# Optimization experiments

Measured on AMD Instinct MI355X. Metric: run time of the kernel, lower is better.

## Reference

```python
import jax, jax.numpy as jnp
import numpy as np

N_NODES = 100000
N_EDGES = 3200000


def gcn_conv(x, edge_index, W, b, n_nodes):
    # PyG GCNConv default: add self-loops, symmetric degree normalization,
    # linear transform, scatter-add aggregation at target nodes, add bias.
    src = jnp.concatenate([edge_index[0], jnp.arange(n_nodes, dtype=edge_index.dtype)])
    dst = jnp.concatenate([edge_index[1], jnp.arange(n_nodes, dtype=edge_index.dtype)])
    deg = jax.ops.segment_sum(jnp.ones_like(dst, dtype=x.dtype), dst, num_segments=n_nodes)
    dinv = jnp.where(deg > 0, jax.lax.rsqrt(jnp.maximum(deg, 1e-12)), 0.0)
    norm = dinv[src] * dinv[dst]            # [E+N]
    h = x @ W                               # [N, F_out]
    msg = h[src] * norm[:, None]            # gather + scale
    out = jax.ops.segment_sum(msg, dst, num_segments=n_nodes)
    return out + b


def setup_inputs() -> dict:
    key = jax.random.key(0)
    k1, k2, k3, k4 = jax.random.split(key, 4)
    x = jax.random.normal(k1, (N_NODES, 2), dtype=jnp.float32)
    edge_index = jax.random.randint(k2, (2, N_EDGES), 0, N_NODES, dtype=jnp.int64)
    # Glorot-ish init for weights, zero bias (PyG default zeros bias).
    W1 = jax.random.normal(k3, (2, 16), dtype=jnp.float32) * (1.0 / np.sqrt(2.0))
    b1 = jnp.zeros((16,), dtype=jnp.float32)
    W2 = jax.random.normal(k4, (16, 2), dtype=jnp.float32) * (1.0 / np.sqrt(16.0))
    b2 = jnp.zeros((2,), dtype=jnp.float32)
    return {"x": x, "edge_index": edge_index, "W1": W1, "b1": b1, "W2": W2, "b2": b2}


def reference(x, edge_index, W1, b1, W2, b2):
    n = x.shape[0]
    h = gcn_conv(x, edge_index, W1, b1, n)
    h = jax.nn.relu(h)
    h = gcn_conv(h, edge_index, W2, b2, n)
    return jax.nn.log_softmax(h, axis=1)
```

## Files before the change

### kernel.cpp

```cpp
#include <hip/hip_runtime.h>
#include <math.h>


#define BLK 256
#define NTILE 512
#define EPTMAX 6400
#define MAXB 512
#define MSK 0x1FFFFu
#define SRTMAX 10240


__global__ void k_hist(const int* __restrict__ dst, int* __restrict__ table,
                       int e, int ept, int nbkt) {
    __shared__ int h[MAXB];
    int tile = blockIdx.x;
    for (int i = threadIdx.x; i < MAXB; i += BLK) h[i] = 0;
    __syncthreads();
    int lo = tile * ept;
    int hi = min(lo + ept, e);
    for (int i = lo + 4 * threadIdx.x; i < hi; i += 4 * BLK) {
        int4 d4 = *(const int4*)(dst + i);
        atomicAdd(&h[d4.x >> 8], 1);
        atomicAdd(&h[d4.y >> 8], 1);
        atomicAdd(&h[d4.z >> 8], 1);
        atomicAdd(&h[d4.w >> 8], 1);
    }
    __syncthreads();
    for (int i = threadIdx.x; i < nbkt; i += BLK)
        table[tile * nbkt + i] = h[i];
}

__global__ void k_scan_col(int* __restrict__ table, int* __restrict__ tot, int nbkt) {
    __shared__ int wsum[NTILE / 64];
    int b = blockIdx.x;
    int t = threadIdx.x;
    int v = table[t * nbkt + b];
    int x = v;
    int lane = t & 63;
#pragma unroll
    for (int ofs = 1; ofs < 64; ofs <<= 1) {
        int y = __shfl_up(x, ofs, 64);
        if (lane >= ofs) x += y;
    }
    if (lane == 63) wsum[t >> 6] = x;
    __syncthreads();
    if (t < NTILE / 64) {
        int s = wsum[t];
        int w = s;
#pragma unroll
        for (int ofs = 1; ofs < NTILE / 64; ofs <<= 1) {
            int y = __shfl_up(w, ofs, 64);
            if (t >= ofs) w += y;
        }
        wsum[t] = w - s;
    }
    __syncthreads();
    int incl = x + wsum[t >> 6];
    table[t * nbkt + b] = incl - v;
    if (t == NTILE - 1) tot[b] = incl;
}

__global__ void k_scan_tot(const int* __restrict__ tot, int* __restrict__ bkt_off, int nbkt) {
    __shared__ int wsum[MAXB / 64];
    int t = threadIdx.x;
    int v = (t < nbkt) ? tot[t] : 0;
    int x = v;
    int lane = t & 63;
#pragma unroll
    for (int ofs = 1; ofs < 64; ofs <<= 1) {
        int y = __shfl_up(x, ofs, 64);
        if (lane >= ofs) x += y;
    }
    if (lane == 63) wsum[t >> 6] = x;
    __syncthreads();
    if (t < MAXB / 64) {
        int s = wsum[t];
        int w = s;
#pragma unroll
        for (int ofs = 1; ofs < MAXB / 64; ofs <<= 1) {
            int y = __shfl_up(w, ofs, 64);
            if (t >= ofs) w += y;
        }
        wsum[t] = w - s;
    }
    __syncthreads();
    int incl = x + wsum[t >> 6];
    if (t < nbkt) bkt_off[t] = incl - v;
    if (t == nbkt - 1) bkt_off[nbkt] = incl;
}

__global__ void k_scatter(const int* __restrict__ src, const int* __restrict__ dst,
                          const int* __restrict__ table, const int* __restrict__ tot,
                          const int* __restrict__ bkt_off, unsigned* __restrict__ sorted,
                          int e, int ept, int nbkt) {
    __shared__ int cur[MAXB];
    __shared__ int base2[MAXB];
    __shared__ unsigned stage[EPTMAX];
    __shared__ unsigned short stage_b[EPTMAX];
    __shared__ int wpart[BLK / 64];
    int tile = blockIdx.x;
    int t = threadIdx.x;
    int lo = tile * ept;
    int hi = min(lo + ept, e);
    int total = hi - lo;

    int b0 = 2 * t, b1 = 2 * t + 1;
    int c0 = 0, c1 = 0, g0 = 0, g1 = 0;
    if (b0 < nbkt) {
        int base = table[tile * nbkt + b0];
        int next = (tile < NTILE - 1) ? table[(tile + 1) * nbkt + b0] : tot[b0];
        c0 = next - base;
        g0 = bkt_off[b0] + base;
    }
    if (b1 < nbkt) {
        int base = table[tile * nbkt + b1];
        int next = (tile < NTILE - 1) ? table[(tile + 1) * nbkt + b1] : tot[b1];
        c1 = next - base;
        g1 = bkt_off[b1] + base;
    }
    int p = c0 + c1;
    int x = p;
    int lane = t & 63;
#pragma unroll
    for (int ofs = 1; ofs < 64; ofs <<= 1) {
        int y = __shfl_up(x, ofs, 64);
        if (lane >= ofs) x += y;
    }
    if (lane == 63) wpart[t >> 6] = x;
    __syncthreads();
    if (t < BLK / 64) {
        int s = wpart[t];
        int w = s;
#pragma unroll
        for (int ofs = 1; ofs < BLK / 64; ofs <<= 1) {
            int y = __shfl_up(w, ofs, 64);
            if (t >= ofs) w += y;
        }
        wpart[t] = w - s;
    }
    __syncthreads();
    int E = x + wpart[t >> 6] - p;
    cur[b0] = E;
    cur[b1] = E + c0;
    if (b0 < nbkt) base2[b0] = g0 - E;
    if (b1 < nbkt) base2[b1] = g1 - (E + c0);
    __syncthreads();

    for (int i = lo + 4 * t; i < hi; i += 4 * BLK) {
        int4 s4 = *(const int4*)(src + i);
        int4 d4 = *(const int4*)(dst + i);
        int b, pos;
        b = d4.x >> 8; pos = atomicAdd(&cur[b], 1);
        stage[pos] = (unsigned)s4.x | ((unsigned)(d4.x & 255) << 17); stage_b[pos] = (unsigned short)b;
        b = d4.y >> 8; pos = atomicAdd(&cur[b], 1);
        stage[pos] = (unsigned)s4.y | ((unsigned)(d4.y & 255) << 17); stage_b[pos] = (unsigned short)b;
        b = d4.z >> 8; pos = atomicAdd(&cur[b], 1);
        stage[pos] = (unsigned)s4.z | ((unsigned)(d4.z & 255) << 17); stage_b[pos] = (unsigned short)b;
        b = d4.w >> 8; pos = atomicAdd(&cur[b], 1);
        stage[pos] = (unsigned)s4.w | ((unsigned)(d4.w & 255) << 17); stage_b[pos] = (unsigned short)b;
    }
    __syncthreads();
    for (int j = t; j < total; j += BLK) {
        int b = stage_b[j];
        sorted[base2[b] + j] = stage[j];
    }
}

__global__ __launch_bounds__(256) void k_cnt(
        const unsigned* __restrict__ sorted, const int* __restrict__ bkt_off,
        const float* __restrict__ x, float* __restrict__ dinv,
        float* __restrict__ xp, int* __restrict__ nodeoff, int n, int nbkt) {
    __shared__ int cnt[256];
    __shared__ int wsum[4];
    int b = blockIdx.x, t = threadIdx.x;
    cnt[t] = 0;
    __syncthreads();
    int lo = bkt_off[b], hi = bkt_off[b + 1];
    int la = lo & ~3;
    for (int i = la + 4 * t; i < hi; i += 4 * 256) {
        uint4 r = *(const uint4*)(sorted + i);
        if (i >= lo && i + 4 <= hi) {
            atomicAdd(&cnt[r.x >> 17], 1);
            atomicAdd(&cnt[r.y >> 17], 1);
            atomicAdd(&cnt[r.z >> 17], 1);
            atomicAdd(&cnt[r.w >> 17], 1);
        } else {
            if (i + 0 >= lo && i + 0 < hi) atomicAdd(&cnt[r.x >> 17], 1);
            if (i + 1 >= lo && i + 1 < hi) atomicAdd(&cnt[r.y >> 17], 1);
            if (i + 2 >= lo && i + 2 < hi) atomicAdd(&cnt[r.z >> 17], 1);
            if (i + 3 >= lo && i + 3 < hi) atomicAdd(&cnt[r.w >> 17], 1);
        }
    }
    __syncthreads();
    int c = cnt[t];
    int node = (b << 8) + t;
    if (node < n) {
        float d = rsqrtf((float)c + 1.0f);
        dinv[node] = d;
        float2 xv = ((const float2*)x)[node];
        ((float2*)xp)[node] = make_float2(d * xv.x, d * xv.y);
    }
    int xsc = c;
    int lane = t & 63;
#pragma unroll
    for (int ofs = 1; ofs < 64; ofs <<= 1) {
        int y = __shfl_up(xsc, ofs, 64);
        if (lane >= ofs) xsc += y;
    }
    if (lane == 63) wsum[t >> 6] = xsc;
    __syncthreads();
    if (t < 4) {
        int s = wsum[t];
        int w = s;
#pragma unroll
        for (int ofs = 1; ofs < 4; ofs <<= 1) {
            int y = __shfl_up(w, ofs, 64);
            if (t >= ofs) w += y;
        }
        wsum[t] = w - s;
    }
    __syncthreads();
    int excl = xsc + wsum[t >> 6] - c;
    nodeoff[node] = lo + excl;
    if (b == nbkt - 1 && t == 255) nodeoff[node + 1] = hi;
}

__global__ __launch_bounds__(1024) void k_sagg1(
        const unsigned* __restrict__ sorted, const int* __restrict__ bkt_off,
        const int* __restrict__ nodeoff, const float* __restrict__ xp,
        const float* __restrict__ dinv, const float* __restrict__ W1,
        const float* __restrict__ b1, const float* __restrict__ W2,
        float* __restrict__ gp, unsigned* __restrict__ nsorted, int n) {
    __shared__ unsigned srt[SRTMAX];
    __shared__ int cur[256];
    __shared__ int stt[257];
    int b = blockIdx.x, t = threadIdx.x;
    int lo = bkt_off[b], hi = bkt_off[b + 1];
    if (t < 256) {
        int s = nodeoff[(b << 8) + t] - lo;
        cur[t] = s;
        stt[t] = s;
        if (t == 255) stt[256] = hi - lo;
    }
    __syncthreads();
    int la = lo & ~3;
    for (int i = la + 4 * t; i < hi; i += 4 * 1024) {
        uint4 r = *(const uint4*)(sorted + i);
        if (i >= lo && i + 4 <= hi) {
            int p0 = atomicAdd(&cur[r.x >> 17], 1); unsigned v0 = r.x & MSK; srt[p0] = v0; nsorted[lo + p0] = v0;
            int p1 = atomicAdd(&cur[r.y >> 17], 1); unsigned v1 = r.y & MSK; srt[p1] = v1; nsorted[lo + p1] = v1;
            int p2 = atomicAdd(&cur[r.z >> 17], 1); unsigned v2 = r.z & MSK; srt[p2] = v2; nsorted[lo + p2] = v2;
            int p3 = atomicAdd(&cur[r.w >> 17], 1); unsigned v3 = r.w & MSK; srt[p3] = v3; nsorted[lo + p3] = v3;
        } else {
            if (i + 0 >= lo && i + 0 < hi) { int p0 = atomicAdd(&cur[r.x >> 17], 1); unsigned v0 = r.x & MSK; srt[p0] = v0; nsorted[lo + p0] = v0; }
            if (i + 1 >= lo && i + 1 < hi) { int p1 = atomicAdd(&cur[r.y >> 17], 1); unsigned v1 = r.y & MSK; srt[p1] = v1; nsorted[lo + p1] = v1; }
            if (i + 2 >= lo && i + 2 < hi) { int p2 = atomicAdd(&cur[r.z >> 17], 1); unsigned v2 = r.z & MSK; srt[p2] = v2; nsorted[lo + p2] = v2; }
            if (i + 3 >= lo && i + 3 < hi) { int p3 = atomicAdd(&cur[r.w >> 17], 1); unsigned v3 = r.w & MSK; srt[p3] = v3; nsorted[lo + p3] = v3; }
        }
    }
    __syncthreads();

    int nl = t >> 2, q = t & 3;
    int gid = (b << 8) + nl;
    int s = stt[nl], epos = stt[nl + 1];
    const float2* xp2 = (const float2*)xp;
    float sx = 0.f, sy = 0.f;
    for (int p = s + q; p < epos; p += 4) {
        float2 f = xp2[srt[p]];
        sx += f.x; sy += f.y;
    }
    sx += __shfl_xor(sx, 1); sy += __shfl_xor(sy, 1);
    sx += __shfl_xor(sx, 2); sy += __shfl_xor(sy, 2);
    if (q == 0 && gid < n) {
        float d = dinv[gid];
        float2 xv = xp2[gid];
        float ax = d * (sx + xv.x), ay = d * (sy + xv.y);
        float g0 = 0.f, g1 = 0.f;
#pragma unroll
        for (int f = 0; f < 16; ++f) {
            float h = fmaf(ax, W1[f], fmaf(ay, W1[16 + f], b1[f]));
            h = fmaxf(h, 0.0f);
            g0 = fmaf(h, W2[2 * f + 0], g0);
            g1 = fmaf(h, W2[2 * f + 1], g1);
        }
        ((float2*)gp)[gid] = make_float2(d * g0, d * g1);
    }
}

__global__ void k_agg2(const unsigned* __restrict__ nsorted, const int* __restrict__ nodeoff,
                       const float* __restrict__ gp, const float* __restrict__ dinv,
                       const float* __restrict__ b2, float* __restrict__ out, int n) {
    int t = threadIdx.x;
    int nd = (blockIdx.x << 8) + (blockIdx.y << 6) + (t >> 2);
    int q = t & 3;
    if (nd >= n) return;
    int start = nodeoff[nd], end = nodeoff[nd + 1];
    const float2* gp2 = (const float2*)gp;
    float sx = 0.f, sy = 0.f;
    for (int p = (start & ~3) + 4 * q; p < end; p += 16) {
        uint4 r = *(const uint4*)(nsorted + p);
        if (p >= start && p + 4 <= end) {
            float2 f0 = gp2[r.x], f1 = gp2[r.y], f2 = gp2[r.z], f3 = gp2[r.w];
            sx += (f0.x + f1.x) + (f2.x + f3.x);
            sy += (f0.y + f1.y) + (f2.y + f3.y);
        } else {
            if (p + 0 >= start && p + 0 < end) { float2 f = gp2[r.x]; sx += f.x; sy += f.y; }
            if (p + 1 >= start && p + 1 < end) { float2 f = gp2[r.y]; sx += f.x; sy += f.y; }
            if (p + 2 >= start && p + 2 < end) { float2 f = gp2[r.z]; sx += f.x; sy += f.y; }
            if (p + 3 >= start && p + 3 < end) { float2 f = gp2[r.w]; sx += f.x; sy += f.y; }
        }
    }
    sx += __shfl_xor(sx, 1); sy += __shfl_xor(sy, 1);
    sx += __shfl_xor(sx, 2); sy += __shfl_xor(sy, 2);
    if (q == 0) {
        float d = dinv[nd];
        float2 gv = gp2[nd];
        float z0 = d * (sx + gv.x) + b2[0];
        float z1 = d * (sy + gv.y) + b2[1];
        float m = fmaxf(z0, z1);
        float lse = m + logf(expf(z0 - m) + expf(z1 - m));
        ((float2*)out)[nd] = make_float2(z0 - lse, z1 - lse);
    }
}

extern "C" void kernel_launch(void* const* d_in, const int* in_sizes, int n_in,
                              void* d_out, int out_size, void* d_ws, size_t ws_size,
                              hipStream_t stream) {
    const float* x  = (const float*)d_in[0];
    const int*   ei = (const int*)d_in[1];
    const float* W1 = (const float*)d_in[2];
    const float* b1 = (const float*)d_in[3];
    const float* W2 = (const float*)d_in[4];
    const float* b2 = (const float*)d_in[5];
    float* out = (float*)d_out;

    const int n = in_sizes[0] / 2;
    const int e = in_sizes[1] / 2;
    const int* src = ei;
    const int* dst = ei + e;

    const int nbkt = (n + 255) >> 8;
    int ept = (((e + NTILE - 1) / NTILE) + 3) & ~3;

    char* base = (char*)d_ws;
    size_t off = 0;
    auto take = [&](size_t bytes) { char* p = base + off; off += (bytes + 255) & ~(size_t)255; return p; };
    unsigned* sorted  = (unsigned*)take(((size_t)e + 8) * 4);
    int*      table   = (int*)take((size_t)NTILE * nbkt * 4);
    int*      tot     = (int*)take((size_t)MAXB * 4);
    int*      bkt_off = (int*)take((size_t)(MAXB + 1) * 4);
    unsigned* nsorted = (unsigned*)take(((size_t)e + 8) * 4);
    int*      nodeoff = (int*)take((size_t)(nbkt * 256 + 64) * 4);
    float*    dinv    = (float*)take((size_t)n * 4);
    float*    xp      = (float*)take((size_t)n * 8);
    float*    gp      = (float*)take((size_t)n * 8);

    dim3 gagg(nbkt, 4);

    k_hist    <<<NTILE, BLK, 0, stream>>>(dst, table, e, ept, nbkt);
    k_scan_col<<<nbkt, NTILE, 0, stream>>>(table, tot, nbkt);
    k_scan_tot<<<1, MAXB, 0, stream>>>(tot, bkt_off, nbkt);
    k_scatter <<<NTILE, BLK, 0, stream>>>(src, dst, table, tot, bkt_off, sorted, e, ept, nbkt);
    k_cnt     <<<nbkt, 256, 0, stream>>>(sorted, bkt_off, x, dinv, xp, nodeoff, n, nbkt);
    k_sagg1   <<<nbkt, 1024, 0, stream>>>(sorted, bkt_off, nodeoff, xp, dinv, W1, b1, W2, gp, nsorted, n);
    k_agg2    <<<gagg, BLK, 0, stream>>>(nsorted, nodeoff, gp, dinv, b2, out, n);
}
```

Measured before the change: 154.3 us.

## Fuse count, layer-1 and layer-2 aggregation into one cooperative kernel

Replaces the three final kernels (degree count, first aggregation with MLP, second aggregation with log-softmax) with one cooperative kernel that uses grid-wide syncs between phases. The per-bucket node-sorted neighbor list stays in shared memory across both layers, so the nsorted global buffer and its re-read are no longer needed, and two kernel launches go away. In exchange it needs all ~391 blocks of 1024 threads to be co-resident and pays for two grid barriers. If the cooperative launch fails it falls back to the old three-kernel path.

```diff
diff --git a/kernel.cpp b/kernel.cpp
--- a/kernel.cpp
+++ b/kernel.cpp
@@ -1,5 +1,8 @@
 #include <hip/hip_runtime.h>
+#include <hip/hip_cooperative_groups.h>
 #include <math.h>
+
+namespace cg = cooperative_groups;
 
 
 #define BLK 256
@@ -165,6 +168,146 @@
         sorted[base2[b] + j] = stage[j];
     }
 }
+
+__global__ __launch_bounds__(1024, 8) void k_fused(
+        const unsigned* __restrict__ sorted, const int* __restrict__ bkt_off,
+        const float* __restrict__ x, float* __restrict__ xp, float* __restrict__ gp,
+        const float* __restrict__ W1, const float* __restrict__ b1,
+        const float* __restrict__ W2, const float* __restrict__ b2,
+        float* __restrict__ out, int n) {
+    __shared__ unsigned srt[SRTMAX];
+    __shared__ int cnt[256];
+    __shared__ int stt[257];
+    __shared__ float dv[256];
+    __shared__ int wsum[4];
+    cg::grid_group grid = cg::this_grid();
+
+    int b = blockIdx.x, t = threadIdx.x;
+    int lo = bkt_off[b], hi = bkt_off[b + 1];
+    if (t < 256) cnt[t] = 0;
+    __syncthreads();
+    int la = lo & ~3;
+
+    for (int i = la + 4 * t; i < hi; i += 4096) {
+        uint4 r = *(const uint4*)(sorted + i);
+        if (i >= lo && i + 4 <= hi) {
+            atomicAdd(&cnt[r.x >> 17], 1);
+            atomicAdd(&cnt[r.y >> 17], 1);
+            atomicAdd(&cnt[r.z >> 17], 1);
+            atomicAdd(&cnt[r.w >> 17], 1);
+        } else {
+            if (i + 0 >= lo && i + 0 < hi) atomicAdd(&cnt[r.x >> 17], 1);
+            if (i + 1 >= lo && i + 1 < hi) atomicAdd(&cnt[r.y >> 17], 1);
+            if (i + 2 >= lo && i + 2 < hi) atomicAdd(&cnt[r.z >> 17], 1);
+            if (i + 3 >= lo && i + 3 < hi) atomicAdd(&cnt[r.w >> 17], 1);
+        }
+    }
+    __syncthreads();
+
+    int c = (t < 256) ? cnt[t] : 0;
+    if (t < 256) {
+        float d = rsqrtf((float)c + 1.0f);
+        dv[t] = d;
+        int node = (b << 8) + t;
+        if (node < n) {
+            float2 xv = ((const float2*)x)[node];
+            ((float2*)xp)[node] = make_float2(d * xv.x, d * xv.y);
+        }
+    }
+    int xsc = c;
+    int lane = t & 63;
+#pragma unroll
+    for (int ofs = 1; ofs < 64; ofs <<= 1) {
+        int y = __shfl_up(xsc, ofs, 64);
+        if (lane >= ofs) xsc += y;
+    }
+    if (t < 256 && lane == 63) wsum[t >> 6] = xsc;
+    __syncthreads();
+    if (t < 4) {
+        int s = wsum[t];
+        int w = s;
+#pragma unroll
+        for (int ofs = 1; ofs < 4; ofs <<= 1) {
+            int y = __shfl_up(w, ofs, 64);
+            if (t >= ofs) w += y;
+        }
+        wsum[t] = w - s;
+    }
+    __syncthreads();
+    if (t < 256) {
+        int excl = xsc + wsum[t >> 6] - c;
+        cnt[t] = excl;
+        stt[t] = excl;
+        if (t == 255) stt[256] = hi - lo;
+    }
+    __syncthreads();
+
+    for (int i = la + 4 * t; i < hi; i += 4096) {
+        uint4 r = *(const uint4*)(sorted + i);
+        if (i >= lo && i + 4 <= hi) {
+            int p0 = atomicAdd(&cnt[r.x >> 17], 1); srt[p0] = r.x & MSK;
+            int p1 = atomicAdd(&cnt[r.y >> 17], 1); srt[p1] = r.y & MSK;
+            int p2 = atomicAdd(&cnt[r.z >> 17], 1); srt[p2] = r.z & MSK;
+            int p3 = atomicAdd(&cnt[r.w >> 17], 1); srt[p3] = r.w & MSK;
+        } else {
+            if (i + 0 >= lo && i + 0 < hi) { int p0 = atomicAdd(&cnt[r.x >> 17], 1); srt[p0] = r.x & MSK; }
+            if (i + 1 >= lo && i + 1 < hi) { int p1 = atomicAdd(&cnt[r.y >> 17], 1); srt[p1] = r.y & MSK; }
+            if (i + 2 >= lo && i + 2 < hi) { int p2 = atomicAdd(&cnt[r.z >> 17], 1); srt[p2] = r.z & MSK; }
+            if (i + 3 >= lo && i + 3 < hi) { int p3 = atomicAdd(&cnt[r.w >> 17], 1); srt[p3] = r.w & MSK; }
+        }
+    }
+
+    __threadfence();
+    grid.sync();
+
+    int nl = t >> 2, q = t & 3;
+    int gid = (b << 8) + nl;
+    int s0 = stt[nl], e0 = stt[nl + 1];
+    const float2* xp2 = (const float2*)xp;
+    float sx = 0.f, sy = 0.f;
+    for (int p = s0 + q; p < e0; p += 4) {
+        float2 f = xp2[srt[p]];
+        sx += f.x; sy += f.y;
+    }
+    sx += __shfl_xor(sx, 1); sy += __shfl_xor(sy, 1);
+    sx += __shfl_xor(sx, 2); sy += __shfl_xor(sy, 2);
+    if (q == 0 && gid < n) {
+        float d = dv[nl];
+        float2 xv = xp2[gid];
+        float ax = d * (sx + xv.x), ay = d * (sy + xv.y);
+        float g0 = 0.f, g1 = 0.f;
+#pragma unroll
+        for (int f = 0; f < 16; ++f) {
+            float h = fmaf(ax, W1[f], fmaf(ay, W1[16 + f], b1[f]));
+            h = fmaxf(h, 0.0f);
+            g0 = fmaf(h, W2[2 * f + 0], g0);
+            g1 = fmaf(h, W2[2 * f + 1], g1);
+        }
+        ((float2*)gp)[gid] = make_float2(d * g0, d * g1);
+    }
+
+    __threadfence();
+    grid.sync();
+
+    const float2* gp2 = (const float2*)gp;
+    float tx = 0.f, ty = 0.f;
+    for (int p = s0 + q; p < e0; p += 4) {
+        float2 f = gp2[srt[p]];
+        tx += f.x; ty += f.y;
+    }
+    tx += __shfl_xor(tx, 1); ty += __shfl_xor(ty, 1);
+    tx += __shfl_xor(tx, 2); ty += __shfl_xor(ty, 2);
+    if (q == 0 && gid < n) {
+        float d = dv[nl];
+        float2 gv = gp2[gid];
+        float z0 = d * (tx + gv.x) + b2[0];
+        float z1 = d * (ty + gv.y) + b2[1];
+        float m = fmaxf(z0, z1);
+        float lse = m + logf(expf(z0 - m) + expf(z1 - m));
+        ((float2*)out)[gid] = make_float2(z0 - lse, z1 - lse);
+    }
+}
+
 
 __global__ __launch_bounds__(256) void k_cnt(
         const unsigned* __restrict__ sorted, const int* __restrict__ bkt_off,
@@ -259,7 +402,6 @@
         }
     }
     __syncthreads();
-
     int nl = t >> 2, q = t & 3;
     int gid = (b << 8) + nl;
     int s = stt[nl], epos = stt[nl + 1];
@@ -355,13 +497,20 @@
     float*    xp      = (float*)take((size_t)n * 8);
     float*    gp      = (float*)take((size_t)n * 8);
 
-    dim3 gagg(nbkt, 4);
-
     k_hist    <<<NTILE, BLK, 0, stream>>>(dst, table, e, ept, nbkt);
     k_scan_col<<<nbkt, NTILE, 0, stream>>>(table, tot, nbkt);
     k_scan_tot<<<1, MAXB, 0, stream>>>(tot, bkt_off, nbkt);
     k_scatter <<<NTILE, BLK, 0, stream>>>(src, dst, table, tot, bkt_off, sorted, e, ept, nbkt);
-    k_cnt     <<<nbkt, 256, 0, stream>>>(sorted, bkt_off, x, dinv, xp, nodeoff, n, nbkt);
-    k_sagg1   <<<nbkt, 1024, 0, stream>>>(sorted, bkt_off, nodeoff, xp, dinv, W1, b1, W2, gp, nsorted, n);
-    k_agg2    <<<gagg, BLK, 0, stream>>>(nsorted, nodeoff, gp, dinv, b2, out, n);
-}
+
+    int nn = n;
+    void* args[] = {(void*)&sorted, (void*)&bkt_off, (void*)&x, (void*)&xp, (void*)&gp,
+                    (void*)&W1, (void*)&b1, (void*)&W2, (void*)&b2, (void*)&out, (void*)&nn};
+    hipError_t cerr = hipLaunchCooperativeKernel((const void*)k_fused, dim3(nbkt), dim3(1024),
+                                                 args, 0, stream);
+    if (cerr != hipSuccess) {
+        dim3 gagg(nbkt, 4);
+        k_cnt  <<<nbkt, 256, 0, stream>>>(sorted, bkt_off, x, dinv, xp, nodeoff, n, nbkt);
+        k_sagg1<<<nbkt, 1024, 0, stream>>>(sorted, bkt_off, nodeoff, xp, dinv, W1, b1, W2, gp, nsorted, n);
+        k_agg2 <<<gagg, BLK, 0, stream>>>(nsorted, nodeoff, gp, dinv, b2, out, n);
+    }
+}
```

New measurement: 439.8 us. 2.85x slower.
